# Kernel tuning notes

Hardware: AMD Instinct MI355X
Metric: run time of the kernel (lower is better)

The kernel has to match this reference:

```python
import jax, jax.numpy as jnp
import numpy as np

B, T, H = 1, 2048, 2048
HEADS, DH = 16, 128  # head_dim = H // HEADS
K = 50               # block size
NEG = -1e9


def setup_inputs() -> dict:
    key = jax.random.key(0)
    ks = jax.random.split(key, 6)
    x = jax.random.normal(ks[0], (B, T, H), jnp.float32)
    mask = jnp.ones((B, T), jnp.float32)
    bias = jax.random.normal(ks[1], (B, HEADS, T, T), jnp.float32) * 0.02
    s = 1.0 / np.sqrt(H)
    Wq = jax.random.normal(ks[2], (H, HEADS, DH), jnp.float32) * s
    Wk = jax.random.normal(ks[3], (H, HEADS, DH), jnp.float32) * s
    Wv = jax.random.normal(ks[4], (H, HEADS, DH), jnp.float32) * s
    Wo = jax.random.normal(ks[5], (HEADS, DH, H), jnp.float32) * (1.0 / np.sqrt(H))
    return {"x_BxTxH": x, "mask_BxT": mask, "attention_bias_BxHxTxT": bias,
            "Wq": Wq, "Wk": Wk, "Wv": Wv, "Wo": Wo}


def _local_self_attention(x, mask, bias, Wq, Wk, Wv, Wo):
    b, t, h = x.shape
    extra = K - t % K          # module always pads (pads a full block if t % K == 0)
    p = t + extra
    n = p // K
    # pad + block the inputs: [b, n, K, h]
    xb = jnp.pad(x, ((0, 0), (0, extra), (0, 0))).reshape(b, n, K, h)
    # pad mask with -1e9 (as in the module), block, build pairwise mask via multiply
    mb = jnp.pad(mask, ((0, 0), (0, extra)), constant_values=NEG).reshape(b, n, K)
    pair = mb[..., :, None] * mb[..., None, :]              # [b, n, K, K]
    mask_bias = jnp.where(pair > 0, 0.0, NEG)[:, :, None]   # [b, n, 1, K, K] (broadcast heads)
    # pad attention bias and extract block-diagonal: [b, n, heads, K, K]
    bp = jnp.pad(bias, ((0, 0), (0, 0), (0, extra), (0, extra)))
    nb = bp.reshape(b, HEADS, n, K, n, K)
    idx = jnp.arange(n)
    blk_bias = nb[:, :, idx, :, idx, :]          # [n, b, heads, K, K]
    blk_bias = jnp.transpose(blk_bias, (1, 0, 2, 3, 4))  # [b, n, heads, K, K]
    # per-block multi-head attention (no qkv bias, query scaled by head_dim**-0.5)
    q = jnp.einsum('bnkh,hef->bnkef', xb, Wq) * (DH ** -0.5)
    k = jnp.einsum('bnkh,hef->bnkef', xb, Wk)
    v = jnp.einsum('bnkh,hef->bnkef', xb, Wv)
    logits = jnp.einsum('bnqef,bnkef->bneqk', q, k) + blk_bias + mask_bias
    attn = jax.nn.softmax(logits, axis=-1)
    out = jnp.einsum('bneqk,bnkef->bnqef', attn, v)
    out = jnp.einsum('bnqef,efh->bnqh', out, Wo).reshape(b, p, h)
    return out[:, :t, :]


def reference(x_BxTxH, mask_BxT, attention_bias_BxHxTxT, Wq, Wk, Wv, Wo):
    return _local_self_attention(x_BxTxH, mask_BxT, attention_bias_BxHxTxT, Wq, Wk, Wv, Wo)
```

## Files before the change

### kernel.cpp

```cpp
#include <hip/hip_runtime.h>
#include <hip/hip_bf16.h>

typedef _Float16 f16x8 __attribute__((ext_vector_type(8)));
typedef float f32x4 __attribute__((ext_vector_type(4)));

#define T_DIM 2048
#define H_DIM 2048
#define N_HEADS 16
#define DH 128
#define KBLK 50
#define NBLK 41
#define NEGV (-1.0e9f)
#define QSCALE 0.08838834764831845f

__device__ __forceinline__ void gl_lds16(const void* g, void* l) {
    __builtin_amdgcn_global_load_lds(
        (const __attribute__((address_space(1))) void*)g,
        (__attribute__((address_space(3))) void*)l, 16, 0, 0);
}

__global__ __launch_bounds__(256) void prep_kernel(const float* __restrict__ x,
                                                   const float* __restrict__ Wq,
                                                   const float* __restrict__ Wk,
                                                   const float* __restrict__ Wv,
                                                   const float* __restrict__ Wo,
                                                   _Float16* __restrict__ xb,
                                                   _Float16* __restrict__ WT,
                                                   _Float16* __restrict__ WoT) {
    __shared__ float tile[32][33];
    int z = blockIdx.z;
    const float* src = (z == 0) ? Wq : (z == 1) ? Wk : (z == 2) ? Wv : (z == 3) ? Wo : x;
    _Float16* dst = (z == 3) ? WoT : (z == 4) ? xb : (WT + (size_t)z * T_DIM * H_DIM);
    int bx = blockIdx.x * 32, by = blockIdx.y * 32;
    int tx = threadIdx.x, ty = threadIdx.y;
    if (z == 4) {
#pragma unroll
        for (int i = 0; i < 4; i++) {
            int r = by + ty + i * 8;
            dst[(size_t)r * H_DIM + bx + tx] = (_Float16)src[(size_t)r * H_DIM + bx + tx];
        }
    } else {
#pragma unroll
        for (int i = 0; i < 4; i++)
            tile[ty + i * 8][tx] = src[(size_t)(by + ty + i * 8) * H_DIM + bx + tx];
        __syncthreads();
#pragma unroll
        for (int i = 0; i < 4; i++)
            dst[(size_t)(bx + ty + i * 8) * H_DIM + by + tx] = (_Float16)tile[tx][ty + i * 8];
    }
}

template <int MODE, int BN>
__global__ __launch_bounds__(256) void gemm_kernel(const _Float16* __restrict__ A,
                                                   const _Float16* __restrict__ BT,
                                                   void* __restrict__ Cout,
                                                   int M, int N, int K) {
    constexpr int BM = 128, BK = 32;
    constexpr int NB = BN / 32;
    __shared__ _Float16 As[2][BM * BK];
    __shared__ _Float16 Bs[2][BN * BK];
    int tid = threadIdx.x;
    int lane = tid & 63, wave = tid >> 6;
    int bm = blockIdx.y * BM, bn = blockIdx.x * BN;
    int wr = (wave >> 1) * 64, wc = (wave & 1) * (BN / 2);
    int cb = lane & 15, hi = lane >> 4;

    f32x4 acc[4][NB];
#pragma unroll
    for (int m = 0; m < 4; m++)
#pragma unroll
        for (int n = 0; n < NB; n++) acc[m][n] = (f32x4){0.f, 0.f, 0.f, 0.f};

    auto stage = [&](int t, int buf) {
        int k0 = t * BK;
#pragma unroll
        for (int r = 0; r < (BM * BK / 8) / 256; r++) {
            int c = tid + r * 256;
            int row = c >> 2, cc = c & 3;
            gl_lds16(&A[(size_t)(bm + row) * K + k0 + cc * 8], &As[buf][c * 8]);
        }
#pragma unroll
        for (int r = 0; r < (BN * BK / 8) / 256; r++) {
            int c = tid + r * 256;
            int row = c >> 2, cc = c & 3;
            gl_lds16(&BT[(size_t)(bn + row) * K + k0 + cc * 8], &Bs[buf][c * 8]);
        }
    };

    const int NT = K / BK;
    stage(0, 0);
    __syncthreads();
    int cur = 0;
    for (int t = 0; t < NT; t++) {
        if (t + 1 < NT) stage(t + 1, cur ^ 1);
        f16x8 a[4], b[NB];
#pragma unroll
        for (int m = 0; m < 4; m++)
            a[m] = *(const f16x8*)&As[cur][(wr + m * 16 + cb) * BK + hi * 8];
#pragma unroll
        for (int n = 0; n < NB; n++)
            b[n] = *(const f16x8*)&Bs[cur][(wc + n * 16 + cb) * BK + hi * 8];
#pragma unroll
        for (int m = 0; m < 4; m++)
#pragma unroll
            for (int n = 0; n < NB; n++)
                acc[m][n] = __builtin_amdgcn_mfma_f32_16x16x32_f16(a[m], b[n], acc[m][n], 0, 0, 0);
        __syncthreads();
        cur ^= 1;
    }

    if (MODE == 0) {
        _Float16* qkv = (_Float16*)Cout;
#pragma unroll
        for (int m = 0; m < 4; m++) {
#pragma unroll
            for (int n = 0; n < NB; n++) {
                int gn = bn + wc + n * 16 + cb;
                int tensor = gn >> 11;
                int ef = gn & 2047;
                int e = ef >> 7, f = ef & 127;
                float scale = (tensor == 0) ? QSCALE : 1.0f;
                _Float16* base = qkv + (size_t)tensor * (T_DIM * H_DIM) + (size_t)e * (T_DIM * DH) + f;
#pragma unroll
                for (int r = 0; r < 4; r++) {
                    int gm = bm + wr + m * 16 + hi * 4 + r;
                    base[(size_t)gm * DH] = (_Float16)(acc[m][n][r] * scale);
                }
            }
        }
    } else {
        float* C = (float*)Cout;
#pragma unroll
        for (int m = 0; m < 4; m++)
#pragma unroll
            for (int n = 0; n < NB; n++) {
                int gn = bn + wc + n * 16 + cb;
#pragma unroll
                for (int r = 0; r < 4; r++) {
                    int gm = bm + wr + m * 16 + hi * 4 + r;
                    C[(size_t)gm * N + gn] = acc[m][n][r];
                }
            }
    }
}

__global__ __launch_bounds__(256) void attn_kernel(const _Float16* __restrict__ qkvb,
                                                   const float* __restrict__ bias,
                                                   const float* __restrict__ mask,
                                                   _Float16* __restrict__ aout) {
    int bid = blockIdx.x;
    int n = bid >> 4, e = bid & 15;
    int t0 = n * KBLK;
    int valid = (T_DIM - t0 < KBLK) ? (T_DIM - t0) : KBLK;

    __shared__ _Float16 Qs[64 * 136];
    __shared__ _Float16 Ks[64 * 136];
    __shared__ _Float16 VTs[128 * 72];
    __shared__ _Float16 Ps[64 * 72];
    __shared__ float maskv[64];

    int tid = threadIdx.x;
    int lane = tid & 63, wave = tid >> 6;
    const _Float16* qp = qkvb + (size_t)e * (T_DIM * DH);
    const _Float16* kp = qkvb + (size_t)(T_DIM * H_DIM) + (size_t)e * (T_DIM * DH);
    const _Float16* vp = qkvb + (size_t)2 * (T_DIM * H_DIM) + (size_t)e * (T_DIM * DH);

#pragma unroll
    for (int i = 0; i < 4; i++) {
        int c = tid + i * 256;
        int r = c >> 4, c8 = c & 15;
        uint4 z = {0u, 0u, 0u, 0u};
        uint4 vq = z, vk = z;
        if (r < valid) {
            vq = *(const uint4*)&qp[(size_t)(t0 + r) * DH + c8 * 8];
            vk = *(const uint4*)&kp[(size_t)(t0 + r) * DH + c8 * 8];
        }
        *(uint4*)&Qs[r * 136 + c8 * 8] = vq;
        *(uint4*)&Ks[r * 136 + c8 * 8] = vk;
    }
#pragma unroll
    for (int i = 0; i < 4; i++) {
        int c = tid + i * 256;
        int r = c & 63;
        int f0 = (c >> 6) * 8;
        uint4 v = {0u, 0u, 0u, 0u};
        if (r < valid) v = *(const uint4*)&vp[(size_t)(t0 + r) * DH + f0];
        _Float16 tmp[8];
        *(uint4*)tmp = v;
#pragma unroll
        for (int j = 0; j < 8; j++) VTs[(f0 + j) * 72 + r] = tmp[j];
    }
    if (tid < 64) maskv[tid] = (tid < valid) ? mask[t0 + tid] : NEGV;
    __syncthreads();

    int qr0 = wave * 16;
    int cb = lane & 15, hi = lane >> 4;

    f16x8 aq[4];
#pragma unroll
    for (int ks = 0; ks < 4; ks++)
        aq[ks] = *(const f16x8*)&Qs[(qr0 + cb) * 136 + ks * 32 + hi * 8];
    f32x4 s[4];
#pragma unroll
    for (int kt = 0; kt < 4; kt++) s[kt] = (f32x4){0.f, 0.f, 0.f, 0.f};
#pragma unroll
    for (int kt = 0; kt < 4; kt++)
#pragma unroll
        for (int ks = 0; ks < 4; ks++) {
            f16x8 bk = *(const f16x8*)&Ks[(kt * 16 + cb) * 136 + ks * 32 + hi * 8];
            s[kt] = __builtin_amdgcn_mfma_f32_16x16x32_f16(aq[ks], bk, s[kt], 0, 0, 0);
        }

#pragma unroll
    for (int r = 0; r < 4; r++) {
        int rl = qr0 + hi * 4 + r;
        int qi = t0 + rl;
        float mq = maskv[rl];
        float lg[4];
        float mx = -3.4e38f;
#pragma unroll
        for (int kt = 0; kt < 4; kt++) {
            int cl = kt * 16 + cb, ki = t0 + cl;
            float bg = (qi < T_DIM && ki < T_DIM)
                           ? bias[((size_t)e * T_DIM + qi) * T_DIM + ki] : 0.f;
            float pr = mq * maskv[cl];
            float v = s[kt][r] + bg + (pr > 0.f ? 0.f : NEGV);
            lg[kt] = v;
            mx = fmaxf(mx, v);
        }
#pragma unroll
        for (int off = 8; off; off >>= 1) mx = fmaxf(mx, __shfl_xor(mx, off));
        float sum = 0.f;
#pragma unroll
        for (int kt = 0; kt < 4; kt++) {
            float pe = __expf(lg[kt] - mx);
            lg[kt] = pe;
            sum += pe;
        }
#pragma unroll
        for (int off = 8; off; off >>= 1) sum += __shfl_xor(sum, off);
        float inv = 1.f / sum;
#pragma unroll
        for (int kt = 0; kt < 4; kt++)
            Ps[rl * 72 + kt * 16 + cb] = (_Float16)(lg[kt] * inv);
    }
    __syncthreads();

    f16x8 pa[2];
#pragma unroll
    for (int ks = 0; ks < 2; ks++)
        pa[ks] = *(const f16x8*)&Ps[(qr0 + cb) * 72 + ks * 32 + hi * 8];
#pragma unroll
    for (int ft = 0; ft < 8; ft++) {
        f32x4 o = (f32x4){0.f, 0.f, 0.f, 0.f};
#pragma unroll
        for (int ks = 0; ks < 2; ks++) {
            f16x8 bv = *(const f16x8*)&VTs[(ft * 16 + cb) * 72 + ks * 32 + hi * 8];
            o = __builtin_amdgcn_mfma_f32_16x16x32_f16(pa[ks], bv, o, 0, 0, 0);
        }
#pragma unroll
        for (int r = 0; r < 4; r++) {
            int rl = qr0 + hi * 4 + r;
            if (rl < valid)
                aout[(size_t)(t0 + rl) * H_DIM + e * DH + ft * 16 + cb] = (_Float16)o[r];
        }
    }
}

extern "C" void kernel_launch(void* const* d_in, const int* in_sizes, int n_in,
                              void* d_out, int out_size, void* d_ws, size_t ws_size,
                              hipStream_t stream) {
    const float* x    = (const float*)d_in[0];
    const float* mask = (const float*)d_in[1];
    const float* bias = (const float*)d_in[2];
    const float* Wq   = (const float*)d_in[3];
    const float* Wk   = (const float*)d_in[4];
    const float* Wv   = (const float*)d_in[5];
    const float* Wo   = (const float*)d_in[6];
    float* out = (float*)d_out;

    _Float16* xb   = (_Float16*)d_ws;
    _Float16* WT   = xb + (size_t)T_DIM * H_DIM;
    _Float16* WoT  = WT + (size_t)3 * T_DIM * H_DIM;
    _Float16* qkvb = WoT + (size_t)T_DIM * H_DIM;
    _Float16* aout = qkvb + (size_t)3 * T_DIM * H_DIM;

    prep_kernel<<<dim3(64, 64, 5), dim3(32, 8), 0, stream>>>(x, Wq, Wk, Wv, Wo, xb, WT, WoT);

    gemm_kernel<0, 128><<<dim3(6144 / 128, T_DIM / 128), 256, 0, stream>>>(
        xb, WT, (void*)qkvb, T_DIM, 3 * H_DIM, H_DIM);

    attn_kernel<<<NBLK * N_HEADS, 256, 0, stream>>>(qkvb, bias, mask, aout);

    gemm_kernel<1, 64><<<dim3(H_DIM / 64, T_DIM / 128), 256, 0, stream>>>(
        aout, WoT, (void*)out, T_DIM, H_DIM, H_DIM);
}
```

Baseline: 141.9 us.

## Triple-buffer GEMM LDS staging with explicit vmcnt waits and one barrier

```diff
diff --git a/kernel.cpp b/kernel.cpp
--- a/kernel.cpp
+++ b/kernel.cpp
@@ -57,8 +57,10 @@
                                                    int M, int N, int K) {
     constexpr int BM = 128, BK = 32;
     constexpr int NB = BN / 32;
-    __shared__ _Float16 As[2][BM * BK];
-    __shared__ _Float16 Bs[2][BN * BK];
+    constexpr int AL = (BM * BK / 8) / 256;
+    constexpr int BL = (BN * BK / 8) / 256;
+    __shared__ _Float16 As[3][BM * BK];
+    __shared__ _Float16 Bs[3][BN * BK];
     int tid = threadIdx.x;
     int lane = tid & 63, wave = tid >> 6;
     int bm = blockIdx.y * BM, bn = blockIdx.x * BN;
@@ -74,40 +76,57 @@
     auto stage = [&](int t, int buf) {
         int k0 = t * BK;
 #pragma unroll
-        for (int r = 0; r < (BM * BK / 8) / 256; r++) {
+        for (int r = 0; r < AL; r++) {
             int c = tid + r * 256;
-            int row = c >> 2, cc = c & 3;
-            gl_lds16(&A[(size_t)(bm + row) * K + k0 + cc * 8], &As[buf][c * 8]);
-        }
-#pragma unroll
-        for (int r = 0; r < (BN * BK / 8) / 256; r++) {
+            gl_lds16(&A[(size_t)(bm + (c >> 2)) * K + k0 + (c & 3) * 8], &As[buf][c * 8]);
+        }
+#pragma unroll
+        for (int r = 0; r < BL; r++) {
             int c = tid + r * 256;
-            int row = c >> 2, cc = c & 3;
-            gl_lds16(&BT[(size_t)(bn + row) * K + k0 + cc * 8], &Bs[buf][c * 8]);
-        }
+            gl_lds16(&BT[(size_t)(bn + (c >> 2)) * K + k0 + (c & 3) * 8], &Bs[buf][c * 8]);
+        }
+    };
+
+    auto compute = [&](int cur) {
+        f16x8 a[4], b[NB];
+#pragma unroll
+        for (int m = 0; m < 4; m++)
+            a[m] = *(const f16x8*)&As[cur][(wr + m * 16 + cb) * BK + hi * 8];
+#pragma unroll
+        for (int n = 0; n < NB; n++)
+            b[n] = *(const f16x8*)&Bs[cur][(wc + n * 16 + cb) * BK + hi * 8];
+#pragma unroll
+        for (int m = 0; m < 4; m++)
+#pragma unroll
+            for (int n = 0; n < NB; n++)
+                acc[m][n] = __builtin_amdgcn_mfma_f32_16x16x32_f16(a[m], b[n], acc[m][n], 0, 0, 0);
     };
 
     const int NT = K / BK;
     stage(0, 0);
-    __syncthreads();
-    int cur = 0;
-    for (int t = 0; t < NT; t++) {
-        if (t + 1 < NT) stage(t + 1, cur ^ 1);
-        f16x8 a[4], b[NB];
-#pragma unroll
-        for (int m = 0; m < 4; m++)
-            a[m] = *(const f16x8*)&As[cur][(wr + m * 16 + cb) * BK + hi * 8];
-#pragma unroll
-        for (int n = 0; n < NB; n++)
-            b[n] = *(const f16x8*)&Bs[cur][(wc + n * 16 + cb) * BK + hi * 8];
-#pragma unroll
-        for (int m = 0; m < 4; m++)
-#pragma unroll
-            for (int n = 0; n < NB; n++)
-                acc[m][n] = __builtin_amdgcn_mfma_f32_16x16x32_f16(a[m], b[n], acc[m][n], 0, 0, 0);
-        __syncthreads();
-        cur ^= 1;
-    }
+    stage(1, 1);
+
+    int cur = 0, nx2 = 2;
+    for (int t = 0; t < NT - 2; t++) {
+        if constexpr (AL + BL == 4)
+            asm volatile("s_waitcnt vmcnt(4) lgkmcnt(0)" ::: "memory");
+        else
+            asm volatile("s_waitcnt vmcnt(3) lgkmcnt(0)" ::: "memory");
+        __builtin_amdgcn_s_barrier();
+        __builtin_amdgcn_sched_barrier(0);
+        stage(t + 2, nx2);
+        compute(cur);
+        cur = (cur == 2) ? 0 : cur + 1;
+        nx2 = (nx2 == 2) ? 0 : nx2 + 1;
+    }
+    asm volatile("s_waitcnt vmcnt(0) lgkmcnt(0)" ::: "memory");
+    __builtin_amdgcn_s_barrier();
+    __builtin_amdgcn_sched_barrier(0);
+    compute(cur);
+    cur = (cur == 2) ? 0 : cur + 1;
+    __builtin_amdgcn_s_barrier();
+    __builtin_amdgcn_sched_barrier(0);
+    compute(cur);
 
     if (MODE == 0) {
         _Float16* qkv = (_Float16*)Cout;
```

Result: no change. 142.9 us (+0.7%).
